# Kernel tuning notes

Measured on AMD Instinct MI355X. Metric: run time of the kernel, lower is better.

The kernel has to match this reference:

```python
import jax, jax.numpy as jnp
import numpy as np

VOCAB, NUM_CLASSES, E, H = 50257, 20, 64, 64
B, T = 128, 2048


def setup_inputs() -> dict:
    key = jax.random.key(0)
    ks = jax.random.split(key, 16)
    s_ih = 1.0 / np.sqrt(H)
    u = lambda k, shape: jax.random.uniform(k, shape, jnp.float32, -s_ih, s_ih)
    return {
        'tokens': jax.random.randint(ks[0], (B, T), 0, VOCAB),
        'emb': jax.random.normal(ks[1], (VOCAB, E), jnp.float32),
        # forward-direction GRU params (PyTorch layout: [3H, *], gate order r,z,n)
        'wih_f': u(ks[2], (3 * H, E)), 'whh_f': u(ks[3], (3 * H, H)),
        'bih_f': u(ks[4], (3 * H,)), 'bhh_f': u(ks[5], (3 * H,)),
        # backward-direction GRU params
        'wih_b': u(ks[6], (3 * H, E)), 'whh_b': u(ks[7], (3 * H, H)),
        'bih_b': u(ks[8], (3 * H,)), 'bhh_b': u(ks[9], (3 * H,)),
        # classifier: Linear(4H -> H), GELU, Linear(H -> C)
        'w1': u(ks[10], (H, 4 * H)), 'b1': u(ks[11], (H,)),
        'w2': u(ks[12], (NUM_CLASSES, H)), 'b2': u(ks[13], (NUM_CLASSES,)),
    }


def _gru_dir(x, wih, whh, bih, bhh):
    # x: [B, T, E] -> outputs [B, T, H]; PyTorch GRU gate math, gates (r, z, n)
    xg = jnp.einsum('bte,ge->tbg', x, wih) + bih  # precompute input projections [T,B,3H]
    h0 = jnp.zeros((x.shape[0], H), x.dtype)

    def step(h, xg_t):
        hg = h @ whh.T + bhh
        xr, xz, xn = jnp.split(xg_t, 3, axis=-1)
        hr, hz, hn = jnp.split(hg, 3, axis=-1)
        r = jax.nn.sigmoid(xr + hr)
        z = jax.nn.sigmoid(xz + hz)
        n = jnp.tanh(xn + r * hn)
        h_new = (1.0 - z) * n + z * h
        return h_new, h_new

    _, hs = jax.lax.scan(step, h0, xg)  # hs: [T, B, H]
    return hs.transpose(1, 0, 2)


def reference(tokens, emb, wih_f, whh_f, bih_f, bhh_f,
              wih_b, whh_b, bih_b, bhh_b, w1, b1, w2, b2):
    x = emb[tokens]  # [B, T, E]
    h_fwd = _gru_dir(x, wih_f, whh_f, bih_f, bhh_f)
    h_bwd = _gru_dir(x[:, ::-1], wih_b, whh_b, bih_b, bhh_b)[:, ::-1]
    encoded = jnp.concatenate([h_fwd, h_bwd], axis=-1)  # [B, T, 2H]
    feats = jnp.concatenate([encoded.mean(axis=1), encoded.max(axis=1)], axis=-1)  # [B, 4H]
    hid = jax.nn.gelu(feats @ w1.T + b1, approximate=False)
    return hid @ w2.T + b2  # [B, C]
```

## Files before the change

### kernel.cpp

```cpp
#include <hip/hip_runtime.h>
#include <hip/hip_bf16.h>
#include <math.h>

#define VOCAB 50257
#define NCLS 20
#define EDIM 64
#define HDIM 64
#define BATCH 128
#define TLEN 2048

typedef float v2f __attribute__((ext_vector_type(2)));

__device__ float g_P[(size_t)2 * VOCAB * 192];
__device__ float g_feats[BATCH * 256];

__device__ __forceinline__ float fast_rcp(float x) { return __builtin_amdgcn_rcpf(x); }

__device__ __forceinline__ float fsigmoid(float x) {
    return fast_rcp(1.f + __expf(-x));
}
__device__ __forceinline__ float ftanh(float x) {
    float e = __expf(2.f * x);
    return 1.f - 2.f * fast_rcp(e + 1.f);
}

__global__ __launch_bounds__(384) void precompute_P(
    const float* __restrict__ emb,
    const float* __restrict__ wih_f, const float* __restrict__ bih_f,
    const float* __restrict__ wih_b, const float* __restrict__ bih_b)
{
    const int t = threadIdx.x;
    const int dir = t / 192;
    const int g = t % 192;
    const float* wih = dir ? wih_b : wih_f;
    const float* bih = dir ? bih_b : bih_f;

    float4 wq0, wq1, wq2, wq3, wq4, wq5, wq6, wq7;
    float4 wq8, wq9, wq10, wq11, wq12, wq13, wq14, wq15;
#define LDWQ(K) wq##K = *(const float4*)(wih + (size_t)g * 64 + 4 * K)
    LDWQ(0); LDWQ(1); LDWQ(2); LDWQ(3); LDWQ(4); LDWQ(5); LDWQ(6); LDWQ(7);
    LDWQ(8); LDWQ(9); LDWQ(10); LDWQ(11); LDWQ(12); LDWQ(13); LDWQ(14); LDWQ(15);
#undef LDWQ
    const float bias = bih[g];
    float* Pd = g_P + (size_t)dir * VOCAB * 192;

    for (int v = blockIdx.x * 2; v < VOCAB; v += gridDim.x * 2) {
        const int v1ok = (v + 1 < VOCAB);
        const float4* e0 = (const float4*)(emb + (size_t)v * 64);
        const float4* e1 = (const float4*)(emb + (size_t)(v1ok ? v + 1 : v) * 64);
        float a0 = bias, a1 = bias;
#define PFMA(K) do {                                   \
            float4 x = e0[K];                          \
            float4 y = e1[K];                          \
            a0 = fmaf(x.x, wq##K.x, a0);               \
            a1 = fmaf(y.x, wq##K.x, a1);               \
            a0 = fmaf(x.y, wq##K.y, a0);               \
            a1 = fmaf(y.y, wq##K.y, a1);               \
            a0 = fmaf(x.z, wq##K.z, a0);               \
            a1 = fmaf(y.z, wq##K.z, a1);               \
            a0 = fmaf(x.w, wq##K.w, a0);               \
            a1 = fmaf(y.w, wq##K.w, a1);               \
        } while (0)
        PFMA(0); PFMA(1); PFMA(2); PFMA(3); PFMA(4); PFMA(5); PFMA(6); PFMA(7);
        PFMA(8); PFMA(9); PFMA(10); PFMA(11); PFMA(12); PFMA(13); PFMA(14); PFMA(15);
#undef PFMA
        Pd[(size_t)v * 192 + g] = a0;
        if (v1ok) Pd[(size_t)(v + 1) * 192 + g] = a1;
    }
}

__global__ __launch_bounds__(192, 1) void gru_seq(
    const int* __restrict__ tokens,
    const float* __restrict__ whh_f, const float* __restrict__ bhh_f,
    const float* __restrict__ whh_b, const float* __restrict__ bhh_b)
{
    const int tid = threadIdx.x;
    const int wid = tid >> 6;
    const int lane = tid & 63;
    const int blk = blockIdx.x;
    const int b = blk >> 1;
    const int dir = blk & 1;
    const float* whh = dir ? whh_b : whh_f;
    const float* bhh = dir ? bhh_b : bhh_f;
    const float* Pd = g_P + (size_t)dir * VOCAB * 192 + wid * 64 + lane;

    __shared__ __align__(16) float h_lds[64];
    __shared__ float r_lds[64];
    __shared__ float z_lds[64];
    __shared__ __align__(16) int tok_lds[TLEN];

    {
        const int4* src = (const int4*)(tokens + (size_t)b * TLEN);
        int4* dst = (int4*)tok_lds;
        for (int t = tid; t < TLEN / 4; t += 192) dst[t] = src[t];
    }

    v2f wa0, wa1, wa2, wa3, wa4, wa5, wa6, wa7, wa8, wa9, wa10, wa11, wa12, wa13, wa14, wa15;
    v2f wb0, wb1, wb2, wb3, wb4, wb5, wb6, wb7, wb8, wb9, wb10, wb11, wb12, wb13, wb14, wb15;
    {
        const float* p = whh + (size_t)(wid * 64 + lane) * 64;
#define LDW(K) do { float4 a_ = *(const float4*)(p + 4 * K);                  \
        wa##K = (v2f){a_.x, a_.y}; wb##K = (v2f){a_.z, a_.w}; } while (0)
        LDW(0); LDW(1); LDW(2); LDW(3); LDW(4); LDW(5); LDW(6); LDW(7);
        LDW(8); LDW(9); LDW(10); LDW(11); LDW(12); LDW(13); LDW(14); LDW(15);
#undef LDW
    }
    const float bias = bhh[wid * 64 + lane];

    if (wid == 2) h_lds[lane] = 0.f;
    float h = 0.f, sum = 0.f, mx = -INFINITY;
    __syncthreads();

    auto tok_at = [&](int s) -> int {
        int ss = s < TLEN ? s : TLEN - 1;
        return tok_lds[dir ? (TLEN - 1 - ss) : ss];
    };

    float x0, x1, x2, x3;
#define GRU_PRE(SL, D) \
    asm volatile("global_load_dword %0, %1, off" : "=v"(x##SL) : "v"(Pd + (size_t)tok_at(D) * 192))
    GRU_PRE(0, 0); GRU_PRE(1, 1); GRU_PRE(2, 2); GRU_PRE(3, 3);

#define DOT(K, A0, A1) do {                                                        \
        float4 h4_ = *(const float4*)(h_lds + 4 * K);                              \
        A0 = __builtin_elementwise_fma((v2f){h4_.x, h4_.y}, wa##K, A0);            \
        A1 = __builtin_elementwise_fma((v2f){h4_.z, h4_.w}, wb##K, A1);            \
    } while (0)

#define GRU_STEP(SL, SB) do {                                                      \
        const int tN_ = tok_at((SB) + 4);    \
        v2f a0 = {0.f, 0.f}, a1 = {0.f, 0.f};                                      \
        DOT(0, a0, a1);  DOT(1, a0, a1);  DOT(2, a0, a1);  DOT(3, a0, a1);         \
        DOT(4, a0, a1);  DOT(5, a0, a1);  DOT(6, a0, a1);  DOT(7, a0, a1);         \
        DOT(8, a0, a1);  DOT(9, a0, a1);  DOT(10, a0, a1); DOT(11, a0, a1);        \
        DOT(12, a0, a1); DOT(13, a0, a1); DOT(14, a0, a1); DOT(15, a0, a1);        \
        float hg = (a0.x + a0.y) + (a1.x + a1.y);                                  \
        if (wid != 2) {                                                            \
                    \
            asm volatile("s_waitcnt vmcnt(3)" : "+v"(x##SL));                      \
            float g_ = fsigmoid(x##SL + hg + bias);                                \
            (wid == 0 ? r_lds : z_lds)[lane] = g_;                                 \
            asm volatile("global_load_dword %0, %1, off"                           \
                         : "=v"(x##SL) : "v"(Pd + (size_t)tN_ * 192));             \
        }                                                                          \
        asm volatile("s_waitcnt lgkmcnt(0)" ::: "memory");   \
        __builtin_amdgcn_s_barrier();                          \
        __builtin_amdgcn_sched_barrier(0);                                         \
        if (wid == 2) {                                                            \
            asm volatile("s_waitcnt vmcnt(3)" : "+v"(x##SL));                      \
            float r_ = r_lds[lane];                                                \
            float z_ = z_lds[lane];                                                \
            float n_ = ftanh(x##SL + r_ * (hg + bias));                            \
            h = fmaf(z_, h - n_, n_);                           \
            sum += h;                                                              \
            mx = fmaxf(mx, h);                                                     \
            h_lds[lane] = h;                                                       \
            asm volatile("global_load_dword %0, %1, off"                           \
                         : "=v"(x##SL) : "v"(Pd + (size_t)tN_ * 192));             \
        }                                                                          \
        asm volatile("s_waitcnt lgkmcnt(0)" ::: "memory");    \
        __builtin_amdgcn_s_barrier();                              \
        __builtin_amdgcn_sched_barrier(0);                                         \
    } while (0)

    for (int s = 0; s < TLEN; s += 4) {
        GRU_STEP(0, s + 0);
        GRU_STEP(1, s + 1);
        GRU_STEP(2, s + 2);
        GRU_STEP(3, s + 3);
    }
    asm volatile("s_waitcnt vmcnt(0)" ::: "memory");

    if (wid == 2) {
        g_feats[b * 256 + dir * 64 + lane] = sum * (1.f / TLEN);
        g_feats[b * 256 + 128 + dir * 64 + lane] = mx;
    }
#undef GRU_PRE
#undef GRU_STEP
#undef DOT
}

__global__ __launch_bounds__(64) void classifier(
    const float* __restrict__ w1, const float* __restrict__ b1,
    const float* __restrict__ w2, const float* __restrict__ b2,
    float* __restrict__ out)
{
    const int b = blockIdx.x;
    const int i = threadIdx.x;
    __shared__ float f[256];
    __shared__ float hid[64];
    for (int c = i; c < 256; c += 64) f[c] = g_feats[b * 256 + c];
    __syncthreads();

    float acc = b1[i];
    const float* wrow = w1 + (size_t)i * 256;
#pragma unroll 16
    for (int c = 0; c < 256; c++) acc = fmaf(f[c], wrow[c], acc);
    hid[i] = acc * 0.5f * (1.f + erff(acc * 0.70710678118654752f));
    __syncthreads();

    if (i < NCLS) {
        float o = b2[i];
        const float* w2r = w2 + (size_t)i * 64;
#pragma unroll
        for (int j = 0; j < 64; j++) o = fmaf(hid[j], w2r[j], o);
        out[b * NCLS + i] = o;
    }
}

extern "C" void kernel_launch(void* const* d_in, const int* in_sizes, int n_in,
                              void* d_out, int out_size, void* d_ws, size_t ws_size,
                              hipStream_t stream) {
    const int*   tokens = (const int*)  d_in[0];
    const float* emb    = (const float*)d_in[1];
    const float* wih_f  = (const float*)d_in[2];
    const float* whh_f  = (const float*)d_in[3];
    const float* bih_f  = (const float*)d_in[4];
    const float* bhh_f  = (const float*)d_in[5];
    const float* wih_b  = (const float*)d_in[6];
    const float* whh_b  = (const float*)d_in[7];
    const float* bih_b  = (const float*)d_in[8];
    const float* bhh_b  = (const float*)d_in[9];
    const float* w1     = (const float*)d_in[10];
    const float* b1     = (const float*)d_in[11];
    const float* w2     = (const float*)d_in[12];
    const float* b2     = (const float*)d_in[13];
    float* out = (float*)d_out;

    precompute_P<<<4096, 384, 0, stream>>>(emb, wih_f, bih_f, wih_b, bih_b);
    gru_seq<<<2 * BATCH, 192, 0, stream>>>(tokens, whh_f, bhh_f, whh_b, bhh_b);
    classifier<<<BATCH, 64, 0, stream>>>(w1, b1, w2, b2, out);
}
```

Measured before the change: 982.0 us.

## Split each GRU recurrent dot product across four lanes with shuffle reduction

The recurrent kernel now uses 768 threads per block instead of 192. Each hidden unit's 64-element dot product is split across 4 lanes of 16 elements each and combined with two xor shuffles. This shortens the serial FMA chain per timestep on the latency-bound recurrence and cuts weight registers per thread. In exchange it adds shuffle latency, 12 waves sharing each barrier, and four times as many redundant gather loads from the precomputed projection table.

Result: no change. 972.8 us (-0.9%).

```diff
diff --git a/kernel.cpp b/kernel.cpp
--- a/kernel.cpp
+++ b/kernel.cpp
@@ -69,20 +69,22 @@
     }
 }
 
-__global__ __launch_bounds__(192, 1) void gru_seq(
+__global__ __launch_bounds__(768, 1) void gru_seq(
     const int* __restrict__ tokens,
     const float* __restrict__ whh_f, const float* __restrict__ bhh_f,
     const float* __restrict__ whh_b, const float* __restrict__ bhh_b)
 {
     const int tid = threadIdx.x;
-    const int wid = tid >> 6;
-    const int lane = tid & 63;
+    const int gate = tid >> 8;
+    const int j = tid & 255;
+    const int u = j >> 2;
+    const int c = j & 3;
     const int blk = blockIdx.x;
     const int b = blk >> 1;
     const int dir = blk & 1;
     const float* whh = dir ? whh_b : whh_f;
     const float* bhh = dir ? bhh_b : bhh_f;
-    const float* Pd = g_P + (size_t)dir * VOCAB * 192 + wid * 64 + lane;
+    const float* Pd = g_P + (size_t)dir * VOCAB * 192 + gate * 64 + u;
 
     __shared__ __align__(16) float h_lds[64];
     __shared__ float r_lds[64];
@@ -92,22 +94,20 @@
     {
         const int4* src = (const int4*)(tokens + (size_t)b * TLEN);
         int4* dst = (int4*)tok_lds;
-        for (int t = tid; t < TLEN / 4; t += 192) dst[t] = src[t];
-    }
-
-    v2f wa0, wa1, wa2, wa3, wa4, wa5, wa6, wa7, wa8, wa9, wa10, wa11, wa12, wa13, wa14, wa15;
-    v2f wb0, wb1, wb2, wb3, wb4, wb5, wb6, wb7, wb8, wb9, wb10, wb11, wb12, wb13, wb14, wb15;
+        for (int t = tid; t < TLEN / 4; t += 768) dst[t] = src[t];
+    }
+
+    v2f w0, w1, w2, w3, w4, w5, w6, w7;
     {
-        const float* p = whh + (size_t)(wid * 64 + lane) * 64;
-#define LDW(K) do { float4 a_ = *(const float4*)(p + 4 * K);                  \
-        wa##K = (v2f){a_.x, a_.y}; wb##K = (v2f){a_.z, a_.w}; } while (0)
-        LDW(0); LDW(1); LDW(2); LDW(3); LDW(4); LDW(5); LDW(6); LDW(7);
-        LDW(8); LDW(9); LDW(10); LDW(11); LDW(12); LDW(13); LDW(14); LDW(15);
-#undef LDW
-    }
-    const float bias = bhh[wid * 64 + lane];
-
-    if (wid == 2) h_lds[lane] = 0.f;
+        const float4* p = (const float4*)(whh + (size_t)(gate * 64 + u) * 64 + c * 16);
+        float4 q0 = p[0]; w0 = (v2f){q0.x, q0.y}; w1 = (v2f){q0.z, q0.w};
+        float4 q1 = p[1]; w2 = (v2f){q1.x, q1.y}; w3 = (v2f){q1.z, q1.w};
+        float4 q2 = p[2]; w4 = (v2f){q2.x, q2.y}; w5 = (v2f){q2.z, q2.w};
+        float4 q3 = p[3]; w6 = (v2f){q3.x, q3.y}; w7 = (v2f){q3.z, q3.w};
+    }
+    const float bias = bhh[gate * 64 + u];
+
+    if (tid < 64) h_lds[tid] = 0.f;
     float h = 0.f, sum = 0.f, mx = -INFINITY;
     __syncthreads();
 
@@ -121,45 +121,50 @@
     asm volatile("global_load_dword %0, %1, off" : "=v"(x##SL) : "v"(Pd + (size_t)tok_at(D) * 192))
     GRU_PRE(0, 0); GRU_PRE(1, 1); GRU_PRE(2, 2); GRU_PRE(3, 3);
 
-#define DOT(K, A0, A1) do {                                                        \
-        float4 h4_ = *(const float4*)(h_lds + 4 * K);                              \
-        A0 = __builtin_elementwise_fma((v2f){h4_.x, h4_.y}, wa##K, A0);            \
-        A1 = __builtin_elementwise_fma((v2f){h4_.z, h4_.w}, wb##K, A1);            \
-    } while (0)
-
 #define GRU_STEP(SL, SB) do {                                                      \
         const int tN_ = tok_at((SB) + 4);    \
+        const float4* hb_ = (const float4*)(h_lds + c * 16);                       \
         v2f a0 = {0.f, 0.f}, a1 = {0.f, 0.f};                                      \
-        DOT(0, a0, a1);  DOT(1, a0, a1);  DOT(2, a0, a1);  DOT(3, a0, a1);         \
-        DOT(4, a0, a1);  DOT(5, a0, a1);  DOT(6, a0, a1);  DOT(7, a0, a1);         \
-        DOT(8, a0, a1);  DOT(9, a0, a1);  DOT(10, a0, a1); DOT(11, a0, a1);        \
-        DOT(12, a0, a1); DOT(13, a0, a1); DOT(14, a0, a1); DOT(15, a0, a1);        \
-        float hg = (a0.x + a0.y) + (a1.x + a1.y);                                  \
-        if (wid != 2) {                                                            \
+        { float4 h4_ = hb_[0];                                                     \
+          a0 = __builtin_elementwise_fma((v2f){h4_.x, h4_.y}, w0, a0);             \
+          a1 = __builtin_elementwise_fma((v2f){h4_.z, h4_.w}, w1, a1); }           \
+        { float4 h4_ = hb_[1];                                                     \
+          a0 = __builtin_elementwise_fma((v2f){h4_.x, h4_.y}, w2, a0);             \
+          a1 = __builtin_elementwise_fma((v2f){h4_.z, h4_.w}, w3, a1); }           \
+        { float4 h4_ = hb_[2];                                                     \
+          a0 = __builtin_elementwise_fma((v2f){h4_.x, h4_.y}, w4, a0);             \
+          a1 = __builtin_elementwise_fma((v2f){h4_.z, h4_.w}, w5, a1); }           \
+        { float4 h4_ = hb_[3];                                                     \
+          a0 = __builtin_elementwise_fma((v2f){h4_.x, h4_.y}, w6, a0);             \
+          a1 = __builtin_elementwise_fma((v2f){h4_.z, h4_.w}, w7, a1); }           \
+        float p_ = (a0.x + a0.y) + (a1.x + a1.y);                                  \
+        float t_ = p_ + __shfl_xor(p_, 1);               \
+        float hg = t_ + __shfl_xor(t_, 2);                                         \
+        if (gate != 2) {                                                           \
                     \
             asm volatile("s_waitcnt vmcnt(3)" : "+v"(x##SL));                      \
             float g_ = fsigmoid(x##SL + hg + bias);                                \
-            (wid == 0 ? r_lds : z_lds)[lane] = g_;                                 \
+            if (c == 0) (gate == 0 ? r_lds : z_lds)[u] = g_;                       \
             asm volatile("global_load_dword %0, %1, off"                           \
                          : "=v"(x##SL) : "v"(Pd + (size_t)tN_ * 192));             \
         }                                                                          \
         asm volatile("s_waitcnt lgkmcnt(0)" ::: "memory");   \
         __builtin_amdgcn_s_barrier();                          \
         __builtin_amdgcn_sched_barrier(0);                                         \
-        if (wid == 2) {                                                            \
+        if (gate == 2) {                                                           \
             asm volatile("s_waitcnt vmcnt(3)" : "+v"(x##SL));                      \
-            float r_ = r_lds[lane];                                                \
-            float z_ = z_lds[lane];                                                \
+            float r_ = r_lds[u];                                                   \
+            float z_ = z_lds[u];                                                   \
             float n_ = ftanh(x##SL + r_ * (hg + bias));                            \
             h = fmaf(z_, h - n_, n_);                           \
             sum += h;                                                              \
             mx = fmaxf(mx, h);                                                     \
-            h_lds[lane] = h;                                                       \
+            if (c == 0) h_lds[u] = h;                                              \
             asm volatile("global_load_dword %0, %1, off"                           \
                          : "=v"(x##SL) : "v"(Pd + (size_t)tN_ * 192));             \
         }                                                                          \
         asm volatile("s_waitcnt lgkmcnt(0)" ::: "memory");    \
-        __builtin_amdgcn_s_barrier();                              \
+        __builtin_amdgcn_s_barrier();                            \
         __builtin_amdgcn_sched_barrier(0);                                         \
     } while (0)
 
@@ -171,13 +176,12 @@
     }
     asm volatile("s_waitcnt vmcnt(0)" ::: "memory");
 
-    if (wid == 2) {
-        g_feats[b * 256 + dir * 64 + lane] = sum * (1.f / TLEN);
-        g_feats[b * 256 + 128 + dir * 64 + lane] = mx;
+    if (gate == 2 && c == 0) {
+        g_feats[b * 256 + dir * 64 + u] = sum * (1.f / TLEN);
+        g_feats[b * 256 + 128 + dir * 64 + u] = mx;
     }
 #undef GRU_PRE
 #undef GRU_STEP
-#undef DOT
 }
 
 __global__ __launch_bounds__(64) void classifier(
@@ -228,6 +232,6 @@
     float* out = (float*)d_out;
 
     precompute_P<<<4096, 384, 0, stream>>>(emb, wih_f, bih_f, wih_b, bih_b);
-    gru_seq<<<2 * BATCH, 192, 0, stream>>>(tokens, whh_f, bhh_f, whh_b, bhh_b);
+    gru_seq<<<2 * BATCH, 768, 0, stream>>>(tokens, whh_f, bhh_f, whh_b, bhh_b);
     classifier<<<BATCH, 64, 0, stream>>>(w1, b1, w2, b2, out);
 }
```
